# Performance work log

Measured on AMD Instinct MI355X. Metric: run time of the kernel, lower is better.

## Reference

```python
import jax, jax.numpy as jnp
import numpy as np

K = 5          # knn_step1 = DenseDilatedKnnGraph(5, 1, ...)
BN_EPS = 1e-5  # torch BatchNorm2d default


def setup_inputs() -> dict:
    key = jax.random.key(0)
    k0, k1, k2 = jax.random.split(key, 3)
    B, C, H, W = 8, 128, 256, 256
    x = jax.random.normal(k0, (B, C, H, W), dtype=jnp.float32)
    # conv_seq params: 3x3 conv (no bias), BN affine, 1x1 conv (no bias)
    w1 = jax.random.normal(k1, (C, C, 3, 3), dtype=jnp.float32) * (1.0 / np.sqrt(C * 9))
    gamma = jnp.ones((C,), dtype=jnp.float32)
    beta = jnp.zeros((C,), dtype=jnp.float32)
    w2 = jax.random.normal(k2, (C, C, 1, 1), dtype=jnp.float32) * (1.0 / np.sqrt(C))
    return {"x": x, "w1": w1, "gamma": gamma, "beta": beta, "w2": w2}


def _forward(x, w1, gamma, beta, w2):
    B, C, H, W = x.shape  # H == W required by the original module
    # x_mean[b, n] = mean_{c,w} x[b,c,n,w] + mean_{c,h} x[b,c,h,n]   (B, N)
    xm = x.mean(axis=(1, 3)) + x.mean(axis=(1, 2))
    # DenseDilatedKnnGraph: L2-normalize along channel dim (C=1 -> sign),
    # pairwise sq-distance, top-k nearest (indices built under no_grad in torch)
    v = xm * 0.5
    s = v / jnp.maximum(jnp.abs(v), 1e-12)              # F.normalize, dim=1, C=1
    dist = (s[:, :, None] - s[:, None, :]) ** 2          # (B, N, N), feature dim 1
    _, nn_idx = jax.lax.top_k(-dist, K)                  # (B, N, K) nearest neighbors
    nn_idx = jax.lax.stop_gradient(nn_idx)
    # batched_index_select: gather node features at neighbor indices
    gathered = jax.vmap(lambda f, i: f[i])(xm, nn_idx)   # (B, N, K)
    gate = jax.nn.sigmoid(gathered.sum(axis=-1))         # (B, N)
    # x3.transpose(1,2) * x + x  ->  broadcast gate over channels and width
    y = gate[:, None, :, None] * x + x                   # (B, C, H, W)
    dn = ("NCHW", "OIHW", "NCHW")
    h = jax.lax.conv_general_dilated(y, w1, (1, 1), "SAME", dimension_numbers=dn)
    # BatchNorm2d, training-mode batch statistics (biased variance)
    mu = h.mean(axis=(0, 2, 3), keepdims=True)
    var = h.var(axis=(0, 2, 3), keepdims=True)
    h = (h - mu) * jax.lax.rsqrt(var + BN_EPS)
    h = h * gamma[None, :, None, None] + beta[None, :, None, None]
    h = jax.nn.relu(h)
    out = jax.lax.conv_general_dilated(h, w2, (1, 1), "SAME", dimension_numbers=dn)
    return out


def reference(x, w1, gamma, beta, w2):
    return _forward(x, w1, gamma, beta, w2)
```

## Files before the change

kernel.cpp:

```cpp
#include <hip/hip_runtime.h>
#include <hip/hip_bf16.h>
#include <math.h>

constexpr int B = 8, C = 128, H = 256, W = 256, NN = 256, KNN = 5;
constexpr int HW = H * W;

constexpr int WS_ROWSUM = 0;
constexpr int WS_COLSUM = 2048;
constexpr int WS_GMUL   = 4096;
constexpr int WS_SCALE  = 6144;
constexpr int WS_BIAS   = 6272;
constexpr int WS_PART   = 8192;
constexpr int WS_WT     = 24576;
constexpr int WS_W2T    = 98304;
constexpr size_t WS_Y_BYTES_OFF = 512 * 1024;

constexpr int Y2P_CS = 258 * 8;
constexpr int Y2P_HS = 16 * Y2P_CS;
constexpr int Y2P_BS = 258 * Y2P_HS;
constexpr size_t Y2P_BYTES = (size_t)B * Y2P_BS * 2;

typedef __attribute__((ext_vector_type(8))) short bf16x8;
typedef __attribute__((ext_vector_type(4))) float f32x4;

union U4 { uint4 q; bf16x8 v; unsigned short u[8]; };

__device__ inline unsigned short f2bf(float f) {
    __hip_bfloat16 h = __float2bfloat16(f);
    return *reinterpret_cast<unsigned short*>(&h);
}
__device__ inline float bf2f(unsigned short u) {
    __hip_bfloat16 h = *reinterpret_cast<__hip_bfloat16*>(&u);
    return __bfloat162float(h);
}

__global__ __launch_bounds__(256) void k_sums(const float* __restrict__ x,
                                              float* __restrict__ ws) {
    const int b = blockIdx.x >> 7;
    const int c = blockIdx.x & 127;
    const int t = threadIdx.x;
    const int wv = t >> 6;
    const float4* p4 = (const float4*)(x + (size_t)(b * C + c) * HW);
    __shared__ float srow[256];
    __shared__ float scol[4][256];
    float ca0 = 0.f, ca1 = 0.f, ca2 = 0.f, ca3 = 0.f;
    for (int it = 0; it < 64; ++it) {
        const float4 v = p4[it * 256 + t];
        ca0 += v.x; ca1 += v.y; ca2 += v.z; ca3 += v.w;
        float s = v.x + v.y + v.z + v.w;
#pragma unroll
        for (int m = 1; m < 64; m <<= 1) s += __shfl_xor(s, m);
        if ((t & 63) == 0) srow[it * 4 + wv] = s;
    }
    const int cb = (t & 63) * 4;
    scol[wv][cb + 0] = ca0;
    scol[wv][cb + 1] = ca1;
    scol[wv][cb + 2] = ca2;
    scol[wv][cb + 3] = ca3;
    __syncthreads();
    atomicAdd(&ws[WS_ROWSUM + b * 256 + t], srow[t]);
    atomicAdd(&ws[WS_COLSUM + b * 256 + t],
              scol[0][t] + scol[1][t] + scol[2][t] + scol[3][t]);
}

__global__ void k_gate(float* __restrict__ ws) {
    const int b = blockIdx.x;
    const int i = threadIdx.x;
    __shared__ float xm[256], sgn[256];
    const float v = ws[WS_ROWSUM + b * 256 + i] * (1.f / 32768.f)
                  + ws[WS_COLSUM + b * 256 + i] * (1.f / 32768.f);
    xm[i] = v;
    const float vv = v * 0.5f;
    sgn[i] = vv / fmaxf(fabsf(vv), 1e-12f);
    __syncthreads();
    const float si = sgn[i];
    float bd[KNN];
    int bi[KNN];
    for (int k = 0; k < KNN; ++k) { bd[k] = 1e30f; bi[k] = 0; }
    for (int j = 0; j < NN; ++j) {
        float d = si - sgn[j];
        d *= d;
        if (d < bd[KNN - 1]) {
            int p = KNN - 1;
            while (p > 0 && bd[p - 1] > d) {
                bd[p] = bd[p - 1];
                bi[p] = bi[p - 1];
                --p;
            }
            bd[p] = d;
            bi[p] = j;
        }
    }
    float gs = 0.f;
    for (int k = 0; k < KNN; ++k) gs += xm[bi[k]];
    const float gate = 1.f / (1.f + expf(-gs));
    ws[WS_GMUL + b * 256 + i] = 1.f + gate;
}

__global__ __launch_bounds__(256) void k_yzero(unsigned short* __restrict__ y) {
    const int id = blockIdx.x * 256 + threadIdx.x;
    const uint4 z = {0u, 0u, 0u, 0u};
    if (id < 66048) {
        const int per = Y2P_HS / 8;
        const int b = id / (2 * per);
        const int r = id % (2 * per);
        const int hp = (r >= per) ? 257 : 0;
        const int off = (r >= per) ? r - per : r;
        *reinterpret_cast<uint4*>(y + (size_t)b * Y2P_BS + (size_t)hp * Y2P_HS + off * 8) = z;
    } else {
        const int id2 = id - 66048;
        const int b = id2 >> 13;
        const int r = id2 & 8191;
        const int hp = (r >> 5) + 1;
        const int c8 = (r >> 1) & 15;
        const int wp = (r & 1) ? 257 : 0;
        *reinterpret_cast<uint4*>(y + (size_t)b * Y2P_BS + (size_t)hp * Y2P_HS
                                  + c8 * Y2P_CS + wp * 8) = z;
    }
}

__global__ __launch_bounds__(256) void k_ygenT(const float* __restrict__ x,
                                               const float* __restrict__ ws,
                                               unsigned short* __restrict__ y) {
    const int b = blockIdx.x >> 8;
    const int h = blockIdx.x & 255;
    const int w = threadIdx.x;
    const float g = ws[WS_GMUL + b * 256 + h];
    const float* xp = x + ((size_t)(b * C) * H + h) * W + w;
    unsigned short* yp = y + (size_t)b * Y2P_BS + (size_t)(h + 1) * Y2P_HS + (w + 1) * 8;
    for (int c8 = 0; c8 < 16; ++c8) {
        U4 pk;
#pragma unroll
        for (int j = 0; j < 8; ++j)
            pk.u[j] = f2bf(xp[(size_t)(c8 * 8 + j) * HW] * g);
        *reinterpret_cast<uint4*>(yp + c8 * Y2P_CS) = pk.q;
    }
}

__global__ void k_wprep(const float* __restrict__ w1, unsigned short* __restrict__ wt) {
    const int e = blockIdx.x * 256 + threadIdx.x;
    const int j = e & 7;
    const int kg = (e >> 3) & 3;
    const int och = (e >> 5) & 127;
    const int s = e >> 12;
    const int c = (s & 3) * 32 + kg * 8 + j;
    const int pos = s >> 2;
    const int ky = pos / 3, kx = pos - ky * 3;
    wt[e] = f2bf(w1[(((size_t)och * C + c) * 3 + ky) * 3 + kx]);
}

__global__ void k_wprep2(const float* __restrict__ w2, unsigned short* __restrict__ w2t) {
    const int e = blockIdx.x * 256 + threadIdx.x;
    const int kk = e & 31;
    const int och = (e >> 5) & 127;
    const int s = e >> 12;
    const int k = s * 32 + kk;
    const int c = k >> 2;
    const int t4 = k & 3;
    const float w = w2[och * C + c];
    const unsigned short hi = f2bf(w);
    w2t[e] = (t4 < 2) ? hi : f2bf(w - bf2f(hi));
}

__global__ __launch_bounds__(256) void k_conv3d(const unsigned short* __restrict__ y2,
                                                const unsigned short* __restrict__ wt,
                                                float* __restrict__ ws,
                                                float* __restrict__ hout) {
    const int bx0 = blockIdx.x;
    const int bx = (bx0 & 7) * 512 + (bx0 >> 3);
    const int whalf = bx & 1;
    const int hrow = (bx >> 1) & 255;
    const int b = bx >> 9;
    const int w0 = whalf * 128;

    const int t = threadIdx.x;
    const int wv = t >> 6;
    const int l = t & 63;
    const int wm = wv >> 1, wn = wv & 1;
    const int lr = l & 15, lq = l >> 4;

    __shared__ float sPart[4][128][2];

    f32x4 acc[4][4];
#pragma unroll
    for (int i = 0; i < 4; ++i)
#pragma unroll
        for (int j = 0; j < 4; ++j) acc[i][j] = (f32x4){0.f, 0.f, 0.f, 0.f};

    const unsigned aoff = (unsigned)((wm * 64 + lr) * 32 + lq * 8);
    const unsigned laneB = (unsigned)(lq * Y2P_CS + (w0 + wn * 64 + lr) * 8);
    const unsigned bbase = (unsigned)(b * Y2P_BS);

    uint4 pa0[4], pb0[4], pa1[4], pb1[4];

    auto loadA = [&](int s, uint4* d) {
        const unsigned so = aoff + (unsigned)(s * 4096);
#pragma unroll
        for (int mf = 0; mf < 4; ++mf)
            d[mf] = *reinterpret_cast<const uint4*>(wt + so + mf * 512);
    };
    auto loadB = [&](int s, uint4* d) {
        const int pos = s >> 2;
        const int ky = pos / 3, kx = pos - ky * 3;
        const int cc = s & 3;
        const unsigned sbase = bbase + (unsigned)((hrow + ky) * Y2P_HS + cc * 4 * Y2P_CS)
                             + laneB + (unsigned)(kx * 8);
#pragma unroll
        for (int nf = 0; nf < 4; ++nf)
            d[nf] = *reinterpret_cast<const uint4*>(y2 + sbase + nf * 128);
    };
    auto mfma16 = [&](uint4* pa, uint4* pb) {
#pragma unroll
        for (int mf = 0; mf < 4; ++mf) {
            U4 am; am.q = pa[mf];
#pragma unroll
            for (int nf = 0; nf < 4; ++nf) {
                U4 bm; bm.q = pb[nf];
                acc[mf][nf] = __builtin_amdgcn_mfma_f32_16x16x32_bf16(
                    am.v, bm.v, acc[mf][nf], 0, 0, 0);
            }
        }
    };

    loadA(0, pa0);
    loadB(0, pb0);
    for (int s = 0; s < 36; s += 2) {
        loadA(s + 1, pa1);
        loadB(s + 1, pb1);
        mfma16(pa0, pb0);
        if (s + 2 < 36) {
            loadA(s + 2, pa0);
            loadB(s + 2, pb0);
        }
        mfma16(pa1, pb1);
    }

#pragma unroll
    for (int mf = 0; mf < 4; ++mf) {
#pragma unroll
        for (int reg = 0; reg < 4; ++reg) {
            const int och = wm * 64 + mf * 16 + lq * 4 + reg;
            float* orow = hout + (((size_t)(b * C + och) * H + hrow) * W) + w0;
#pragma unroll
            for (int nf = 0; nf < 4; ++nf)
                orow[wn * 64 + nf * 16 + lr] = acc[mf][nf][reg];
        }
    }

#pragma unroll
    for (int mf = 0; mf < 4; ++mf) {
#pragma unroll
        for (int reg = 0; reg < 4; ++reg) {
            float s = 0.f, q = 0.f;
#pragma unroll
            for (int nf = 0; nf < 4; ++nf) {
                const float v = acc[mf][nf][reg];
                s += v;
                q = fmaf(v, v, q);
            }
#pragma unroll
            for (int m = 1; m < 16; m <<= 1) {
                s += __shfl_xor(s, m);
                q += __shfl_xor(q, m);
            }
            if (lr == 0) {
                const int och = wm * 64 + mf * 16 + lq * 4 + reg;
                sPart[wv][och][0] = s;
                sPart[wv][och][1] = q;
            }
        }
    }
    __syncthreads();
    {
        const int o = t & 127;
        const int which = t >> 7;
        const int wmn = o >> 6;
        const float v = sPart[wmn * 2][o][which] + sPart[wmn * 2 + 1][o][which];
        atomicAdd(&ws[WS_PART + o * 128 + (bx & 63) * 2 + which], v);
    }
}

__device__ inline bf16x8 b_fetch(const float* __restrict__ x, int b, int s,
                                 int hrow, int w0, int px, int kg,
                                 float g0, float g1, float g2) {
    const int pos = s >> 2;
    const int ky = pos / 3, kx = pos - ky * 3;
    const int cbase = (s & 3) * 32 + kg * 8;
    int crow = hrow + ky - 1;
    int col = w0 + px + kx - 1;
    const float g = (ky == 0) ? g0 : ((ky == 1) ? g1 : g2);
    const float sc = ((unsigned)col < (unsigned)W) ? g : 0.f;
    crow = min(max(crow, 0), H - 1);
    col = min(max(col, 0), W - 1);
    const float* p = x + (((size_t)(b * C + cbase) * H + crow) * W + col);
    union { bf16x8 v8; unsigned short u[8]; } r;
#pragma unroll
    for (int j = 0; j < 8; ++j) r.u[j] = f2bf(p[(size_t)j * HW] * sc);
    return r.v8;
}

__global__ __launch_bounds__(256) void k_conv3(const float* __restrict__ x,
                                               const unsigned short* __restrict__ wt,
                                               float* __restrict__ ws,
                                               float* __restrict__ hout) {
    const int bx = blockIdx.x;
    const int whalf = bx & 1;
    const int hrow = (bx >> 1) & 255;
    const int b = bx >> 9;
    const int w0 = whalf * 128;

    const int t = threadIdx.x;
    const int wv = t >> 6;
    const int l = t & 63;
    const int wm = wv >> 1, wn = wv & 1;
    const int lr = l & 15, lq = l >> 4;

    __shared__ unsigned short sA[128 * 40];
    __shared__ unsigned short sB[128 * 40];
    __shared__ float sPart[4][128][2];

    float g0, g1, g2;
    {
        const int r0 = hrow - 1, r2 = hrow + 1;
        g0 = (r0 >= 0) ? ws[WS_GMUL + b * 256 + r0] : 0.f;
        g1 = ws[WS_GMUL + b * 256 + hrow];
        g2 = (r2 < H) ? ws[WS_GMUL + b * 256 + r2] : 0.f;
    }

    f32x4 acc[4][4];
#pragma unroll
    for (int i = 0; i < 4; ++i)
#pragma unroll
        for (int j = 0; j < 4; ++j) acc[i][j] = (f32x4){0.f, 0.f, 0.f, 0.f};

    const int a_och = t & 127, a_h = t >> 7;
    const int b_px = t & 127, b_kg0 = t >> 7;
    const int b_kg1 = b_kg0 + 2;

    uint4 pa0, pa1;
    bf16x8 pb0, pb1;
    {
        const uint4* asrc = reinterpret_cast<const uint4*>(wt + (size_t)a_och * 32 + a_h * 16);
        pa0 = asrc[0];
        pa1 = asrc[1];
        pb0 = b_fetch(x, b, 0, hrow, w0, b_px, b_kg0, g0, g1, g2);
        pb1 = b_fetch(x, b, 0, hrow, w0, b_px, b_kg1, g0, g1, g2);
    }

    for (int s = 0; s < 36; ++s) {
        __syncthreads();
        *reinterpret_cast<uint4*>(&sA[a_och * 40 + a_h * 16]) = pa0;
        *reinterpret_cast<uint4*>(&sA[a_och * 40 + a_h * 16 + 8]) = pa1;
        *reinterpret_cast<bf16x8*>(&sB[b_px * 40 + b_kg0 * 8]) = pb0;
        *reinterpret_cast<bf16x8*>(&sB[b_px * 40 + b_kg1 * 8]) = pb1;
        __syncthreads();

        if (s + 1 < 36) {
            const uint4* asrc = reinterpret_cast<const uint4*>(
                wt + (size_t)(s + 1) * 4096 + (size_t)a_och * 32 + a_h * 16);
            pa0 = asrc[0];
            pa1 = asrc[1];
            pb0 = b_fetch(x, b, s + 1, hrow, w0, b_px, b_kg0, g0, g1, g2);
            pb1 = b_fetch(x, b, s + 1, hrow, w0, b_px, b_kg1, g0, g1, g2);
        }

        bf16x8 af[4], bfr[4];
#pragma unroll
        for (int mf = 0; mf < 4; ++mf) {
            const int och = wm * 64 + mf * 16 + lr;
            af[mf] = *reinterpret_cast<const bf16x8*>(&sA[och * 40 + lq * 8]);
        }
#pragma unroll
        for (int nf = 0; nf < 4; ++nf) {
            const int px = wn * 64 + nf * 16 + lr;
            bfr[nf] = *reinterpret_cast<const bf16x8*>(&sB[px * 40 + lq * 8]);
        }
#pragma unroll
        for (int mf = 0; mf < 4; ++mf)
#pragma unroll
            for (int nf = 0; nf < 4; ++nf)
                acc[mf][nf] = __builtin_amdgcn_mfma_f32_16x16x32_bf16(
                    af[mf], bfr[nf], acc[mf][nf], 0, 0, 0);
    }

#pragma unroll
    for (int mf = 0; mf < 4; ++mf) {
#pragma unroll
        for (int reg = 0; reg < 4; ++reg) {
            const int och = wm * 64 + mf * 16 + lq * 4 + reg;
            float* orow = hout + (((size_t)(b * C + och) * H + hrow) * W) + w0;
#pragma unroll
            for (int nf = 0; nf < 4; ++nf)
                orow[wn * 64 + nf * 16 + lr] = acc[mf][nf][reg];
        }
    }

#pragma unroll
    for (int mf = 0; mf < 4; ++mf) {
#pragma unroll
        for (int reg = 0; reg < 4; ++reg) {
            float s = 0.f, q = 0.f;
#pragma unroll
            for (int nf = 0; nf < 4; ++nf) {
                const float v = acc[mf][nf][reg];
                s += v;
                q = fmaf(v, v, q);
            }
#pragma unroll
            for (int m = 1; m < 16; m <<= 1) {
                s += __shfl_xor(s, m);
                q += __shfl_xor(q, m);
            }
            if (lr == 0) {
                const int och = wm * 64 + mf * 16 + lq * 4 + reg;
                sPart[wv][och][0] = s;
                sPart[wv][och][1] = q;
            }
        }
    }
    __syncthreads();
    {
        const int o = t & 127;
        const int which = t >> 7;
        const int wmn = o >> 6;
        const float v = sPart[wmn * 2][o][which] + sPart[wmn * 2 + 1][o][which];
        atomicAdd(&ws[WS_PART + o * 128 + (bx & 63) * 2 + which], v);
    }
}

__global__ void k_scalebias(const float* __restrict__ gamma,
                            const float* __restrict__ beta, float* __restrict__ ws) {
    const int c = threadIdx.x;
    const float* p = ws + WS_PART + c * 128;
    float s = 0.f, q = 0.f;
    for (int i = 0; i < 64; ++i) {
        s += p[i * 2];
        q += p[i * 2 + 1];
    }
    const float cnt = (float)B * HW;
    const float mu = s / cnt;
    const float var = q / cnt - mu * mu;
    const float rs = rsqrtf(var + 1e-5f);
    const float sc = rs * gamma[c];
    ws[WS_SCALE + c] = sc;
    ws[WS_BIAS + c] = beta[c] - mu * sc;
}

__global__ __launch_bounds__(256) void k_conv1d(float* __restrict__ io,
                                                const unsigned short* __restrict__ w2t,
                                                const float* __restrict__ ws) {
    const int bx = blockIdx.x;
    const int pblk = bx & 511;
    const int b = bx >> 9;
    const size_t p0 = (size_t)pblk * 128;

    const int t = threadIdx.x;
    const int wv = t >> 6;
    const int l = t & 63;
    const int wm = wv >> 1, wn = wv & 1;
    const int lr = l & 15, lq = l >> 4;

    __shared__ float sSB[128][2];
    if (t < 128) {
        sSB[t][0] = ws[WS_SCALE + t];
        sSB[t][1] = ws[WS_BIAS + t];
    }
    __syncthreads();

    f32x4 acc[4][4];
#pragma unroll
    for (int i = 0; i < 4; ++i)
#pragma unroll
        for (int j = 0; j < 4; ++j) acc[i][j] = (f32x4){0.f, 0.f, 0.f, 0.f};

    const unsigned aoff = (unsigned)((wm * 64 + lr) * 32 + lq * 8);
    const float* hplane = io + (size_t)b * C * HW;
    const unsigned vbase = (unsigned)(p0 + wn * 64 + lr);

    uint4 pa0[4], pb0[4], pa1[4], pb1[4];

    auto loadA = [&](int s, uint4* d) {
        const unsigned so = aoff + (unsigned)(s * 4096);
#pragma unroll
        for (int mf = 0; mf < 4; ++mf)
            d[mf] = *reinterpret_cast<const uint4*>(w2t + so + mf * 512);
    };
    auto loadB = [&](int s, uint4* d) {
        const int c0 = s * 8 + lq * 2;
        const float s0 = sSB[c0][0], o0 = sSB[c0][1];
        const float s1 = sSB[c0 + 1][0], o1 = sSB[c0 + 1][1];
        const unsigned off0 = (unsigned)c0 * (unsigned)HW + vbase;
#pragma unroll
        for (int nf = 0; nf < 4; ++nf) {
            const float v0 = fmaxf(fmaf(hplane[off0 + nf * 16], s0, o0), 0.f);
            const float v1 = fmaxf(fmaf(hplane[off0 + HW + nf * 16], s1, o1), 0.f);
            const unsigned short hi0 = f2bf(v0);
            const unsigned short lo0 = f2bf(v0 - bf2f(hi0));
            const unsigned short hi1 = f2bf(v1);
            const unsigned short lo1 = f2bf(v1 - bf2f(hi1));
            U4 fr;
            fr.u[0] = hi0; fr.u[1] = lo0; fr.u[2] = hi0; fr.u[3] = lo0;
            fr.u[4] = hi1; fr.u[5] = lo1; fr.u[6] = hi1; fr.u[7] = lo1;
            d[nf] = fr.q;
        }
    };
    auto mfma16 = [&](uint4* pa, uint4* pb) {
#pragma unroll
        for (int mf = 0; mf < 4; ++mf) {
            U4 am; am.q = pa[mf];
#pragma unroll
            for (int nf = 0; nf < 4; ++nf) {
                U4 bm; bm.q = pb[nf];
                acc[mf][nf] = __builtin_amdgcn_mfma_f32_16x16x32_bf16(
                    am.v, bm.v, acc[mf][nf], 0, 0, 0);
            }
        }
    };

    loadA(0, pa0);
    loadB(0, pb0);
    for (int s = 0; s < 16; s += 2) {
        loadA(s + 1, pa1);
        loadB(s + 1, pb1);
        mfma16(pa0, pb0);
        if (s + 2 < 16) {
            loadA(s + 2, pa0);
            loadB(s + 2, pb0);
        }
        mfma16(pa1, pb1);
    }

    __syncthreads();

#pragma unroll
    for (int mf = 0; mf < 4; ++mf) {
#pragma unroll
        for (int reg = 0; reg < 4; ++reg) {
            const int och = wm * 64 + mf * 16 + lq * 4 + reg;
            float* orow = io + (size_t)(b * C + och) * HW + p0;
#pragma unroll
            for (int nf = 0; nf < 4; ++nf)
                orow[wn * 64 + nf * 16 + lr] = acc[mf][nf][reg];
        }
    }
}

extern "C" void kernel_launch(void* const* d_in, const int* in_sizes, int n_in,
                              void* d_out, int out_size, void* d_ws, size_t ws_size,
                              hipStream_t stream) {
    const float* x = (const float*)d_in[0];
    const float* w1 = (const float*)d_in[1];
    const float* gamma = (const float*)d_in[2];
    const float* beta = (const float*)d_in[3];
    const float* w2 = (const float*)d_in[4];
    float* out = (float*)d_out;
    float* ws = (float*)d_ws;
    unsigned short* wt = (unsigned short*)(ws + WS_WT);
    unsigned short* w2t = (unsigned short*)(ws + WS_W2T);

    hipMemsetAsync(d_ws, 0, 98304, stream);
    k_wprep<<<576, 256, 0, stream>>>(w1, wt);
    k_wprep2<<<256, 256, 0, stream>>>(w2, w2t);
    k_sums<<<B * C, 256, 0, stream>>>(x, ws);
    k_gate<<<B, 256, 0, stream>>>(ws);

    if (ws_size >= WS_Y_BYTES_OFF + Y2P_BYTES) {
        unsigned short* y2 = (unsigned short*)((char*)d_ws + WS_Y_BYTES_OFF);
        k_yzero<<<514, 256, 0, stream>>>(y2);
        k_ygenT<<<B * H, 256, 0, stream>>>(x, ws, y2);
        k_conv3d<<<B * 256 * 2, 256, 0, stream>>>(y2, wt, ws, out);
    } else {
        k_conv3<<<B * 256 * 2, 256, 0, stream>>>(x, wt, ws, out);
    }

    k_scalebias<<<1, 128, 0, stream>>>(gamma, beta, ws);
    k_conv1d<<<B * 512, 256, 0, stream>>>(out, w2t, ws);
}
```

Before: 606.4 us.

## Stage conv3x3 operands through LDS via global_load_lds instead of register prefetch

The 3x3 conv kernel now copies the weight and activation tiles for each K-step into shared memory using direct global-to-LDS loads, then reads the MFMA fragments from LDS. It replaces the previous register double-buffered prefetch, where each wave loaded its own fragments straight from global memory. The aim is to cut redundant global fetches across waves and register pressure. In exchange there is no double buffering and two __syncthreads per step, so load latency is exposed.

```diff
diff --git a/kernel.cpp b/kernel.cpp
--- a/kernel.cpp
+++ b/kernel.cpp
@@ -24,6 +24,12 @@
 typedef __attribute__((ext_vector_type(4))) float f32x4;
 
 union U4 { uint4 q; bf16x8 v; unsigned short u[8]; };
+
+typedef const __attribute__((address_space(1))) unsigned char* gas1;
+typedef __attribute__((address_space(3))) unsigned char* las3;
+__device__ __forceinline__ void gl_lds16(const void* g, void* l) {
+    __builtin_amdgcn_global_load_lds((gas1)g, (las3)l, 16, 0, 0);
+}
 
 __device__ inline unsigned short f2bf(float f) {
     __hip_bfloat16 h = __float2bfloat16(f);
@@ -162,7 +168,7 @@
     w2t[e] = (t4 < 2) ? hi : f2bf(w - bf2f(hi));
 }
 
-__global__ __launch_bounds__(256) void k_conv3d(const unsigned short* __restrict__ y2,
+__global__ __launch_bounds__(256) void k_conv3g(const unsigned short* __restrict__ y2,
                                                 const unsigned short* __restrict__ wt,
                                                 float* __restrict__ ws,
                                                 float* __restrict__ hout) {
@@ -179,6 +185,8 @@
     const int wm = wv >> 1, wn = wv & 1;
     const int lr = l & 15, lq = l >> 4;
 
+    __shared__ __attribute__((aligned(16))) unsigned short sA[4096];
+    __shared__ __attribute__((aligned(16))) unsigned short sB[4096];
     __shared__ float sPart[4][128][2];
 
     f32x4 acc[4][4];
@@ -187,52 +195,45 @@
 #pragma unroll
         for (int j = 0; j < 4; ++j) acc[i][j] = (f32x4){0.f, 0.f, 0.f, 0.f};
 
-    const unsigned aoff = (unsigned)((wm * 64 + lr) * 32 + lq * 8);
-    const unsigned laneB = (unsigned)(lq * Y2P_CS + (w0 + wn * 64 + lr) * 8);
-    const unsigned bbase = (unsigned)(b * Y2P_BS);
-
-    uint4 pa0[4], pb0[4], pa1[4], pb1[4];
-
-    auto loadA = [&](int s, uint4* d) {
-        const unsigned so = aoff + (unsigned)(s * 4096);
+    const char* wtb = (const char*)wt;
+    const char* y2b = (const char*)y2 + (size_t)b * Y2P_BS * 2;
+    const unsigned aLane = (unsigned)(wv * 1024 + l * 16);
+    const int pxl = wv * 16 + (l >> 2);
+    const int k16 = l & 3;
+    const unsigned bLane0 = (unsigned)((pxl * 8 + k16 * Y2P_CS) * 2);
+    const unsigned bLane1 = (unsigned)(((pxl + 64) * 8 + k16 * Y2P_CS) * 2);
+    char* sAp = (char*)sA;
+    char* sBp = (char*)sB;
+
+    const unsigned short* aRd = sA + (wm * 64 + lr) * 32 + lq * 8;
+    const unsigned short* bRd = sB + (wn * 64 + lr) * 32 + lq * 8;
+
+    for (int s = 0; s < 36; ++s) {
+        const int pos = s >> 2, cc = s & 3;
+        const int ky = pos / 3, kx = pos - 3 * ky;
+        const char* aSrc = wtb + ((size_t)s << 13);
+        const char* bSrc = y2b + (size_t)((hrow + ky) * Y2P_HS + cc * 4 * Y2P_CS
+                                          + (w0 + kx) * 8) * 2;
+        gl_lds16(aSrc + aLane,        sAp + wv * 1024);
+        gl_lds16(aSrc + 4096 + aLane, sAp + 4096 + wv * 1024);
+        gl_lds16(bSrc + bLane0,       sBp + wv * 1024);
+        gl_lds16(bSrc + bLane1,       sBp + 4096 + wv * 1024);
+        __syncthreads();
+
+        bf16x8 af[4], bfr[4];
 #pragma unroll
         for (int mf = 0; mf < 4; ++mf)
-            d[mf] = *reinterpret_cast<const uint4*>(wt + so + mf * 512);
-    };
-    auto loadB = [&](int s, uint4* d) {
-        const int pos = s >> 2;
-        const int ky = pos / 3, kx = pos - ky * 3;
-        const int cc = s & 3;
-        const unsigned sbase = bbase + (unsigned)((hrow + ky) * Y2P_HS + cc * 4 * Y2P_CS)
-                             + laneB + (unsigned)(kx * 8);
+            af[mf] = *reinterpret_cast<const bf16x8*>(aRd + mf * 512);
 #pragma unroll
         for (int nf = 0; nf < 4; ++nf)
-            d[nf] = *reinterpret_cast<const uint4*>(y2 + sbase + nf * 128);
-    };
-    auto mfma16 = [&](uint4* pa, uint4* pb) {
-#pragma unroll
-        for (int mf = 0; mf < 4; ++mf) {
-            U4 am; am.q = pa[mf];
-#pragma unroll
-            for (int nf = 0; nf < 4; ++nf) {
-                U4 bm; bm.q = pb[nf];
+            bfr[nf] = *reinterpret_cast<const bf16x8*>(bRd + nf * 512);
+#pragma unroll
+        for (int mf = 0; mf < 4; ++mf)
+#pragma unroll
+            for (int nf = 0; nf < 4; ++nf)
                 acc[mf][nf] = __builtin_amdgcn_mfma_f32_16x16x32_bf16(
-                    am.v, bm.v, acc[mf][nf], 0, 0, 0);
-            }
-        }
-    };
-
-    loadA(0, pa0);
-    loadB(0, pb0);
-    for (int s = 0; s < 36; s += 2) {
-        loadA(s + 1, pa1);
-        loadB(s + 1, pb1);
-        mfma16(pa0, pb0);
-        if (s + 2 < 36) {
-            loadA(s + 2, pa0);
-            loadB(s + 2, pb0);
-        }
-        mfma16(pa1, pb1);
+                    af[mf], bfr[nf], acc[mf][nf], 0, 0, 0);
+        __syncthreads();
     }
 
 #pragma unroll
@@ -568,7 +569,7 @@
         unsigned short* y2 = (unsigned short*)((char*)d_ws + WS_Y_BYTES_OFF);
         k_yzero<<<514, 256, 0, stream>>>(y2);
         k_ygenT<<<B * H, 256, 0, stream>>>(x, ws, y2);
-        k_conv3d<<<B * 256 * 2, 256, 0, stream>>>(y2, wt, ws, out);
+        k_conv3g<<<B * 256 * 2, 256, 0, stream>>>(y2, wt, ws, out);
     } else {
         k_conv3<<<B * 256 * 2, 256, 0, stream>>>(x, wt, ws, out);
     }
```

Result: slower. 622.1 us (+2.6%).
